# Performance work log

Hardware: AMD Instinct MI355X
Metric: run time of the kernel (lower is better)

## Reference

```python
import jax, jax.numpy as jnp
import numpy as np

B, S, D, H = 4, 1024, 1024, 16
HD = D // H
EPS = 1e-5


def _layernorm(x, g, b):
    m = jnp.mean(x, axis=-1, keepdims=True)
    v = jnp.mean((x - m) ** 2, axis=-1, keepdims=True)
    return (x - m) * jax.lax.rsqrt(v + EPS) * g + b


def setup_inputs() -> dict:
    key = jax.random.key(0)
    ks = jax.random.split(key, 8)
    sc = 1.0 / np.sqrt(D)
    return {
        "x": jax.random.normal(ks[0], (B, S, D), dtype=jnp.float32),
        "seq_len": jax.random.randint(ks[1], (B,), 1, S + 1, dtype=jnp.int32),
        "Wq": jax.random.normal(ks[2], (D, D), dtype=jnp.float32) * sc,
        "bq": jnp.zeros((D,), dtype=jnp.float32),
        "Wk": jax.random.normal(ks[3], (D, D), dtype=jnp.float32) * sc,
        "bk": jnp.zeros((D,), dtype=jnp.float32),
        "Wv": jax.random.normal(ks[4], (D, D), dtype=jnp.float32) * sc,
        "bv": jnp.zeros((D,), dtype=jnp.float32),
        "ln_g": jnp.ones((HD,), dtype=jnp.float32),
        "ln_b": jnp.zeros((HD,), dtype=jnp.float32),
    }


def reference(x, seq_len, Wq, bq, Wk, bk, Wv, bv, ln_g, ln_b):
    # Faithful quirk: k and v are projections of the ALREADY projected q.
    q = x @ Wq.T + bq                      # [B,S,D]
    k = q @ Wk.T + bk
    v = q @ Wv.T + bv
    # [B,S,D] -> [B,H,S,HD]
    def split_heads(t):
        return t.reshape(B, S, H, HD).transpose(0, 2, 1, 3)
    q, k, v = split_heads(q), split_heads(k), split_heads(v)
    # shared per-head LayerNorm over head_dim
    q = _layernorm(q, ln_g, ln_b)
    k = _layernorm(k, ln_g, ln_b)
    v = _layernorm(v, ln_g, ln_b)
    # raw scores (no temperature scaling in the original; temperature=1.0 unused)
    scores = jnp.einsum("bhqd,bhkd->bhqk", q, k)
    # encoder_mask: multiplicative validity mask on key positions, repeated per head
    mask = (jnp.arange(S)[None, :] < seq_len[:, None]).astype(scores.dtype)  # [B,S]
    scores = scores * mask[:, None, None, :]
    attn = jax.nn.softmax(scores, axis=-1)
    # dropout is identity at inference
    out = jnp.einsum("bhqk,bhkd->bhqd", attn, v)
    return out.transpose(0, 2, 1, 3).reshape(B, S, D)
```

## Files before the change

kernel.cpp:

```cpp
#include <hip/hip_runtime.h>

#define B_  4
#define S_  1024
#define D_  1024
#define H_  16
#define HD_ 64
#define EPS_ 1e-5f

typedef _Float16 f16x8 __attribute__((ext_vector_type(8)));
typedef _Float16 f16x4 __attribute__((ext_vector_type(4)));
typedef __bf16 bf16x8 __attribute__((ext_vector_type(8)));
typedef float  f32x4  __attribute__((ext_vector_type(4)));
typedef unsigned short ushort8v __attribute__((ext_vector_type(8)));

static __device__ __forceinline__ unsigned short f2bf(float f) {
  union { float f; unsigned u; } v; v.f = f;
  unsigned r = v.u + 0x7fffu + ((v.u >> 16) & 1u);
  return (unsigned short)(r >> 16);
}
static __device__ __forceinline__ float bf2f(unsigned short u) {
  union { unsigned u; float f; } v; v.u = ((unsigned)u) << 16;
  return v.f;
}

#define GLD16(gp, lp) __builtin_amdgcn_global_load_lds( \
    (const __attribute__((address_space(1))) void*)(gp), \
    (__attribute__((address_space(3))) void*)(lp), 16, 0, 0)

__global__ __launch_bounds__(256) void cvt_all(
    const float* __restrict__ x,  _Float16* __restrict__ xh,
    const float* __restrict__ Wq, _Float16* __restrict__ wqh,
    const float* __restrict__ Wk, _Float16* __restrict__ wkh,
    const float* __restrict__ Wv, _Float16* __restrict__ wvh,
    float* __restrict__ Vtail) {
  int bid = blockIdx.x;
  if (bid >= 7168) {
    int i = (bid - 7168) * 1024 + threadIdx.x * 4;
    *(float4*)(Vtail + i) = make_float4(0.f, 0.f, 0.f, 0.f);
    return;
  }
  const float* src; _Float16* dst; int base;
  if (bid < 4096)      { src = x;  dst = xh;  base = bid; }
  else if (bid < 5120) { src = Wq; dst = wqh; base = bid - 4096; }
  else if (bid < 6144) { src = Wk; dst = wkh; base = bid - 5120; }
  else                 { src = Wv; dst = wvh; base = bid - 6144; }
  int i = base * 1024 + threadIdx.x * 4;
  float4 f = *(const float4*)(src + i);
  f16x4 h;
  h.x = (_Float16)f.x; h.y = (_Float16)f.y; h.z = (_Float16)f.z; h.w = (_Float16)f.w;
  *(f16x4*)(dst + i) = h;
}

__global__ __launch_bounds__(256, 2) void gemm_bt_bias(
    const _Float16* __restrict__ A,
    const _Float16* __restrict__ B0, const float* __restrict__ bias0,
    _Float16* __restrict__ C0,
    const _Float16* __restrict__ B1, const float* __restrict__ bias1,
    _Float16* __restrict__ C1,
    int M, int N, int K)
{
  const _Float16* Bm = blockIdx.z ? B1 : B0;
  const float* bias  = blockIdx.z ? bias1 : bias0;
  _Float16* C        = blockIdx.z ? C1 : C0;

  __shared__ _Float16 As[2 * 128 * 32];
  __shared__ _Float16 Bs[2 * 64 * 32];

  int tid  = threadIdx.x;
  int lane = tid & 63;
  int wave = tid >> 6;
  int wm = wave >> 1, wn = wave & 1;
  int qd = lane >> 4, l15 = lane & 15;

  long row0 = (long)blockIdx.y * 128;
  long col0 = (long)blockIdx.x * 64;

  int r_a = tid >> 2;
  int c_a = (tid & 3) * 8;

  f32x4 acc[4][2] = {};

  for (int kk = 0; kk < K; kk += 64) {
    GLD16(A  + (row0 + r_a) * K + kk + c_a,           As + tid * 8);
    GLD16(A  + (row0 + 64 + r_a) * K + kk + c_a,      As + 2048 + tid * 8);
    GLD16(A  + (row0 + r_a) * K + kk + 32 + c_a,      As + 4096 + tid * 8);
    GLD16(A  + (row0 + 64 + r_a) * K + kk + 32 + c_a, As + 6144 + tid * 8);
    GLD16(Bm + (col0 + r_a) * K + kk + c_a,           Bs + tid * 8);
    GLD16(Bm + (col0 + r_a) * K + kk + 32 + c_a,      Bs + 2048 + tid * 8);
    __syncthreads();

    for (int ks = 0; ks < 2; ks++) {
      f16x8 af[4], bfr[2];
      for (int t = 0; t < 4; t++)
        af[t]  = *(const f16x8*)(As + ks * 4096 + (wm * 64 + t * 16 + l15) * 32 + qd * 8);
      for (int j = 0; j < 2; j++)
        bfr[j] = *(const f16x8*)(Bs + ks * 2048 + (wn * 32 + j * 16 + l15) * 32 + qd * 8);
      for (int i = 0; i < 4; i++)
        for (int j = 0; j < 2; j++)
          acc[i][j] = __builtin_amdgcn_mfma_f32_16x16x32_f16(af[i], bfr[j], acc[i][j], 0, 0, 0);
    }
    __syncthreads();
  }

  for (int i = 0; i < 4; i++) {
    long row = row0 + wm * 64 + i * 16 + qd * 4;
    for (int j = 0; j < 2; j++) {
      long col = col0 + wn * 32 + j * 16 + l15;
      float bv = bias[col];
      for (int r = 0; r < 4; r++)
        C[(row + r) * N + col] = (_Float16)(acc[i][j][r] + bv);
    }
  }
}

__global__ __launch_bounds__(256, 2) void gemm_bt_bias128(
    const _Float16* __restrict__ A,
    const _Float16* __restrict__ B0, const float* __restrict__ bias0,
    _Float16* __restrict__ C0,
    const _Float16* __restrict__ B1, const float* __restrict__ bias1,
    _Float16* __restrict__ C1,
    int M, int N, int K)
{
  const _Float16* Bm = blockIdx.z ? B1 : B0;
  const float* bias  = blockIdx.z ? bias1 : bias0;
  _Float16* C        = blockIdx.z ? C1 : C0;

  __shared__ _Float16 As[2 * 128 * 32];
  __shared__ _Float16 Bs[2 * 128 * 32];

  int tid  = threadIdx.x;
  int lane = tid & 63;
  int wave = tid >> 6;
  int wm = wave >> 1, wn = wave & 1;
  int qd = lane >> 4, l15 = lane & 15;

  long row0 = (long)blockIdx.y * 128;
  long col0 = (long)blockIdx.x * 128;

  int r_a = tid >> 2;
  int c_a = (tid & 3) * 8;

  f32x4 acc[4][4] = {};

  for (int kk = 0; kk < K; kk += 64) {
    GLD16(A  + (row0 + r_a) * K + kk + c_a,           As + tid * 8);
    GLD16(A  + (row0 + 64 + r_a) * K + kk + c_a,      As + 2048 + tid * 8);
    GLD16(A  + (row0 + r_a) * K + kk + 32 + c_a,      As + 4096 + tid * 8);
    GLD16(A  + (row0 + 64 + r_a) * K + kk + 32 + c_a, As + 6144 + tid * 8);
    GLD16(Bm + (col0 + r_a) * K + kk + c_a,           Bs + tid * 8);
    GLD16(Bm + (col0 + 64 + r_a) * K + kk + c_a,      Bs + 2048 + tid * 8);
    GLD16(Bm + (col0 + r_a) * K + kk + 32 + c_a,      Bs + 4096 + tid * 8);
    GLD16(Bm + (col0 + 64 + r_a) * K + kk + 32 + c_a, Bs + 6144 + tid * 8);
    __syncthreads();

    for (int ks = 0; ks < 2; ks++) {
      f16x8 af[4], bfr[4];
      for (int t = 0; t < 4; t++) {
        af[t]  = *(const f16x8*)(As + ks * 4096 + (wm * 64 + t * 16 + l15) * 32 + qd * 8);
        bfr[t] = *(const f16x8*)(Bs + ks * 4096 + (wn * 64 + t * 16 + l15) * 32 + qd * 8);
      }
      for (int i = 0; i < 4; i++)
        for (int j = 0; j < 4; j++)
          acc[i][j] = __builtin_amdgcn_mfma_f32_16x16x32_f16(af[i], bfr[j], acc[i][j], 0, 0, 0);
    }
    __syncthreads();
  }

  for (int i = 0; i < 4; i++) {
    long row = row0 + wm * 64 + i * 16 + qd * 4;
    for (int j = 0; j < 4; j++) {
      long col = col0 + wn * 64 + j * 16 + l15;
      float bv = bias[col];
      for (int r = 0; r < 4; r++)
        C[(row + r) * N + col] = (_Float16)(acc[i][j][r] + bv);
    }
  }
}

__global__ __launch_bounds__(256, 2) void ln_qkv(
    const _Float16* __restrict__ qh,
    const _Float16* __restrict__ kh,
    const _Float16* __restrict__ vh,
    const float* __restrict__ ln_g, const float* __restrict__ ln_b,
    const int* __restrict__ seq_len,
    _Float16* __restrict__ Qn,
    _Float16* __restrict__ Kn,
    unsigned short* __restrict__ Vt,
    float* __restrict__ Vtail)
{
  __shared__ unsigned short Vls[256][68];
  int tid = threadIdx.x;
  int s0 = blockIdx.x * 256;
  int h = blockIdx.y, b = blockIdx.z;
  long bh = (long)b * H_ + h;
  long s = s0 + tid;
  long inbase  = ((long)b * S_ + s) * D_ + (long)h * HD_;
  long outbase = (bh * S_ + s) * HD_;

  f16x8 rw[8];
  {
    for (int i = 0; i < 8; i++) rw[i] = *(const f16x8*)(qh + inbase + i * 8);
    float sum = 0.f, sq = 0.f;
    for (int i = 0; i < 8; i++)
      for (int j = 0; j < 8; j++) { float xv = (float)rw[i][j]; sum += xv; sq = fmaf(xv, xv, sq); }
    float m = sum * (1.f / 64.f);
    float inv = rsqrtf(sq * (1.f / 64.f) - m * m + EPS_);
    for (int i = 0; i < 8; i++) {
      f16x8 o;
      for (int j = 0; j < 8; j++)
        o[j] = (_Float16)(((float)rw[i][j] - m) * inv * ln_g[i * 8 + j] + ln_b[i * 8 + j]);
      *(f16x8*)(Qn + outbase + i * 8) = o;
    }
  }
  {
    for (int i = 0; i < 8; i++) rw[i] = *(const f16x8*)(kh + inbase + i * 8);
    float sum = 0.f, sq = 0.f;
    for (int i = 0; i < 8; i++)
      for (int j = 0; j < 8; j++) { float xv = (float)rw[i][j]; sum += xv; sq = fmaf(xv, xv, sq); }
    float m = sum * (1.f / 64.f);
    float inv = rsqrtf(sq * (1.f / 64.f) - m * m + EPS_);
    for (int i = 0; i < 8; i++) {
      f16x8 o;
      for (int j = 0; j < 8; j++)
        o[j] = (_Float16)(((float)rw[i][j] - m) * inv * ln_g[i * 8 + j] + ln_b[i * 8 + j]);
      *(f16x8*)(Kn + outbase + i * 8) = o;
    }
  }
  {
    for (int i = 0; i < 8; i++) rw[i] = *(const f16x8*)(vh + inbase + i * 8);
    float sum = 0.f, sq = 0.f;
    for (int i = 0; i < 8; i++)
      for (int j = 0; j < 8; j++) { float xv = (float)rw[i][j]; sum += xv; sq = fmaf(xv, xv, sq); }
    float m = sum * (1.f / 64.f);
    float inv = rsqrtf(sq * (1.f / 64.f) - m * m + EPS_);
    for (int i = 0; i < 8; i++)
      for (int j = 0; j < 8; j++)
        Vls[tid][i * 8 + j] = f2bf(((float)rw[i][j] - m) * inv * ln_g[i * 8 + j] + ln_b[i * 8 + j]);
  }
  __syncthreads();
  int d = tid >> 2, sc = tid & 3;
  int len = seq_len[b];
  long vbase = (bh * HD_ + d) * S_ + s0 + sc * 64;
  float tsum = 0.f;
  for (int j0 = 0; j0 < 64; j0 += 8) {
    ushort8v w;
    for (int jj = 0; jj < 8; jj++) {
      unsigned short ub = Vls[sc * 64 + j0 + jj][d];
      w[jj] = ub;
      if (s0 + sc * 64 + j0 + jj >= len) tsum += bf2f(ub);
    }
    *(ushort8v*)(Vt + vbase + j0) = w;
  }
  if (s0 + sc * 64 + 64 > len)
    atomicAdd(&Vtail[bh * HD_ + d], tsum);
}

__global__ __launch_bounds__(256, 2) void attn(
    const _Float16* __restrict__ Qn,
    const _Float16* __restrict__ Kn,
    const unsigned short* __restrict__ Vt,
    const float* __restrict__ Vtail,
    const int* __restrict__ seq_len,
    float* __restrict__ out)
{
  __shared__ _Float16 Ks[2][64 * 32];
  __shared__ unsigned short Vts[2][64 * 32];
  __shared__ unsigned short Ps[4][32 * 72];

  int tid = threadIdx.x, lane = tid & 63, wave = tid >> 6;
  int qd = lane >> 4, l15 = lane & 15;
  int b = blockIdx.x;
  int h = blockIdx.y;
  int q0 = blockIdx.z * 128;
  long bh = (long)b * H_ + h;
  int len = seq_len[b];
  int ntile = (len + 63) >> 6;

  int skey = tid >> 2;
  int schunk = (tid & 3) * 8;

  f16x8 qf[2][2];
  for (int mt = 0; mt < 2; mt++) {
    const _Float16* qp = Qn + (bh * S_ + q0 + wave * 32 + mt * 16 + l15) * HD_;
    qf[mt][0] = *(const f16x8*)(qp + qd * 8);
    qf[mt][1] = *(const f16x8*)(qp + 32 + qd * 8);
  }
  float tv[4];
  for (int t = 0; t < 4; t++) tv[t] = Vtail[bh * HD_ + t * 16 + l15];

  f32x4 o[2][4] = {};
  float den[2][4] = {{0.f,0.f,0.f,0.f},{0.f,0.f,0.f,0.f}};

  for (int kt = 0; kt < ntile; kt++) {
    GLD16(Kn + (bh * S_ + kt * 64 + skey) * HD_ + schunk,      &Ks[0][0] + tid * 8);
    GLD16(Kn + (bh * S_ + kt * 64 + skey) * HD_ + 32 + schunk, &Ks[1][0] + tid * 8);
    GLD16(Vt + (bh * HD_ + skey) * S_ + kt * 64 + schunk,      &Vts[0][0] + tid * 8);
    GLD16(Vt + (bh * HD_ + skey) * S_ + kt * 64 + 32 + schunk, &Vts[1][0] + tid * 8);
    __syncthreads();

    f32x4 sacc[2][4] = {};
    for (int tn = 0; tn < 4; tn++) {
      f16x8 kf0 = *(const f16x8*)(&Ks[0][0] + (tn * 16 + l15) * 32 + qd * 8);
      f16x8 kf1 = *(const f16x8*)(&Ks[1][0] + (tn * 16 + l15) * 32 + qd * 8);
      for (int mt = 0; mt < 2; mt++) {
        sacc[mt][tn] = __builtin_amdgcn_mfma_f32_16x16x32_f16(qf[mt][0], kf0, sacc[mt][tn], 0, 0, 0);
        sacc[mt][tn] = __builtin_amdgcn_mfma_f32_16x16x32_f16(qf[mt][1], kf1, sacc[mt][tn], 0, 0, 0);
      }
    }

    for (int mt = 0; mt < 2; mt++)
      for (int tn = 0; tn < 4; tn++) {
        int kg = kt * 64 + tn * 16 + l15;
        for (int r = 0; r < 4; r++) {
          float p = (kg < len) ? __expf(sacc[mt][tn][r]) : 0.f;
          unsigned short pb = f2bf(p);
          den[mt][r] += bf2f(pb);
          Ps[wave][(mt * 16 + qd * 4 + r) * 72 + tn * 16 + l15] = pb;
        }
      }

    bf16x8 pf[2][2];
    for (int mt = 0; mt < 2; mt++) {
      pf[mt][0] = *(const bf16x8*)(&Ps[wave][(mt * 16 + l15) * 72 + qd * 8]);
      pf[mt][1] = *(const bf16x8*)(&Ps[wave][(mt * 16 + l15) * 72 + 32 + qd * 8]);
    }
    for (int t = 0; t < 4; t++) {
      bf16x8 vf0 = *(const bf16x8*)(&Vts[0][0] + (t * 16 + l15) * 32 + qd * 8);
      bf16x8 vf1 = *(const bf16x8*)(&Vts[1][0] + (t * 16 + l15) * 32 + qd * 8);
      for (int mt = 0; mt < 2; mt++) {
        o[mt][t] = __builtin_amdgcn_mfma_f32_16x16x32_bf16(pf[mt][0], vf0, o[mt][t], 0, 0, 0);
        o[mt][t] = __builtin_amdgcn_mfma_f32_16x16x32_bf16(pf[mt][1], vf1, o[mt][t], 0, 0, 0);
      }
    }
    __syncthreads();
  }

  for (int mt = 0; mt < 2; mt++)
    for (int t = 0; t < 4; t++)
      for (int r = 0; r < 4; r++) o[mt][t][r] += tv[t];

  float tden = (float)(S_ - len);
  for (int mt = 0; mt < 2; mt++)
    for (int r = 0; r < 4; r++) {
      for (int off = 1; off < 16; off <<= 1)
        den[mt][r] += __shfl_xor(den[mt][r], off, 64);
      den[mt][r] += tden;
    }

  for (int mt = 0; mt < 2; mt++)
    for (int t = 0; t < 4; t++)
      for (int r = 0; r < 4; r++) {
        long s = q0 + wave * 32 + mt * 16 + qd * 4 + r;
        long dcol = (long)h * HD_ + t * 16 + l15;
        out[((long)b * S_ + s) * D_ + dcol] = o[mt][t][r] / den[mt][r];
      }
}

extern "C" void kernel_launch(void* const* d_in, const int* in_sizes, int n_in,
                              void* d_out, int out_size, void* d_ws, size_t ws_size,
                              hipStream_t stream) {
  const float* x     = (const float*)d_in[0];
  const int*  seq    = (const int*)d_in[1];
  const float* Wq    = (const float*)d_in[2];
  const float* bq    = (const float*)d_in[3];
  const float* Wk    = (const float*)d_in[4];
  const float* bk    = (const float*)d_in[5];
  const float* Wv    = (const float*)d_in[6];
  const float* bv    = (const float*)d_in[7];
  const float* ln_g  = (const float*)d_in[8];
  const float* ln_b  = (const float*)d_in[9];
  float* out = (float*)d_out;

  char* ws = (char*)d_ws;
  _Float16* xh  = (_Float16*)(ws);
  _Float16* wqh = (_Float16*)(ws + (8l  << 20));
  _Float16* wkh = (_Float16*)(ws + (10l << 20));
  _Float16* wvh = (_Float16*)(ws + (12l << 20));
  float*    Vtail = (float*)(ws + (14l << 20));
  _Float16* qh  = (_Float16*)(ws + (16l << 20));
  _Float16* kh  = (_Float16*)(ws + (24l << 20));
  _Float16* vh  = (_Float16*)(ws + (32l << 20));
  _Float16* Qn  = (_Float16*)(ws + (40l << 20));
  _Float16* Kn  = (_Float16*)(ws + (48l << 20));
  unsigned short* Vt = (unsigned short*)(ws + (56l << 20));

  cvt_all<<<7172, 256, 0, stream>>>(x, xh, Wq, wqh, Wk, wkh, Wv, wvh, Vtail);

  dim3 g1(D_ / 64, (B_ * S_) / 128, 1);
  gemm_bt_bias<<<g1, 256, 0, stream>>>(xh, wqh, bq, qh, wqh, bq, qh,
                                       B_ * S_, D_, D_);
  dim3 g2(D_ / 128, (B_ * S_) / 128, 2);
  gemm_bt_bias128<<<g2, 256, 0, stream>>>(qh, wkh, bk, kh, wvh, bv, vh,
                                          B_ * S_, D_, D_);

  dim3 g3(S_ / 256, H_, B_);
  ln_qkv<<<g3, 256, 0, stream>>>(qh, kh, vh, ln_g, ln_b, seq, Qn, Kn, Vt, Vtail);

  dim3 g4(B_, H_, S_ / 128);
  attn<<<g4, 256, 0, stream>>>(Qn, Kn, Vt, Vtail, seq, out);
}
```

Baseline: 181.7 us.

## Split LN over 4 lanes per row with coalesced LDS-staged loads

Rewrites the per-head LayerNorm kernel so each row is handled by four lanes with shuffle reductions instead of one thread per row, and stages the Q/K/V tiles through shared memory using coalesced 16-byte async loads. Blocks now cover 64 sequence positions rather than 256, giving 4x more blocks and a higher occupancy hint. The aim is to raise parallelism and memory coalescing in a bandwidth-bound stage. In exchange it adds more blocks, more atomics on Vtail, and extra LDS traffic.

```diff
diff --git a/kernel.cpp b/kernel.cpp
--- a/kernel.cpp
+++ b/kernel.cpp
@@ -177,7 +177,7 @@
   }
 }
 
-__global__ __launch_bounds__(256, 2) void ln_qkv(
+__global__ __launch_bounds__(256, 4) void ln_qkv(
     const _Float16* __restrict__ qh,
     const _Float16* __restrict__ kh,
     const _Float16* __restrict__ vh,
@@ -188,70 +188,116 @@
     unsigned short* __restrict__ Vt,
     float* __restrict__ Vtail)
 {
-  __shared__ unsigned short Vls[256][68];
-  int tid = threadIdx.x;
-  int s0 = blockIdx.x * 256;
+  __shared__ _Float16 Qs[2][64 * 32];
+  __shared__ _Float16 Ks_[2][64 * 32];
+  __shared__ _Float16 Vs[2][64 * 32];
+  __shared__ unsigned short Vls[64][68];
+
+  int tid = threadIdx.x, lane = tid & 63, w = tid >> 6;
+  int a = lane >> 4, r16 = lane & 15;
+  int row = w * 16 + r16;
+  int s0 = blockIdx.x * 64;
   int h = blockIdx.y, b = blockIdx.z;
   long bh = (long)b * H_ + h;
-  long s = s0 + tid;
-  long inbase  = ((long)b * S_ + s) * D_ + (long)h * HD_;
-  long outbase = (bh * S_ + s) * HD_;
-
-  f16x8 rw[8];
+  int len = seq_len[b];
+
+  int skey = tid >> 2, schunk = (tid & 3) * 8;
+  long gbase = ((long)b * S_ + s0 + skey) * D_ + (long)h * HD_ + schunk;
+  GLD16(qh + gbase,      &Qs[0][0] + tid * 8);
+  GLD16(qh + gbase + 32, &Qs[1][0] + tid * 8);
+  GLD16(kh + gbase,      &Ks_[0][0] + tid * 8);
+  GLD16(kh + gbase + 32, &Ks_[1][0] + tid * 8);
+  GLD16(vh + gbase,      &Vs[0][0] + tid * 8);
+  GLD16(vh + gbase + 32, &Vs[1][0] + tid * 8);
+
+  float g0[8], bb0[8], g1[8], bb1[8];
+  for (int u = 0; u < 8; u++) {
+    g0[u] = ln_g[a * 8 + u];       bb0[u] = ln_b[a * 8 + u];
+    g1[u] = ln_g[32 + a * 8 + u];  bb1[u] = ln_b[32 + a * 8 + u];
+  }
+  __syncthreads();
+
+  long obase = (bh * S_ + s0 + row) * HD_;
+
   {
-    for (int i = 0; i < 8; i++) rw[i] = *(const f16x8*)(qh + inbase + i * 8);
+    f16x8 x0 = *(const f16x8*)(&Qs[0][row * 32 + a * 8]);
+    f16x8 x1 = *(const f16x8*)(&Qs[1][row * 32 + a * 8]);
     float sum = 0.f, sq = 0.f;
-    for (int i = 0; i < 8; i++)
-      for (int j = 0; j < 8; j++) { float xv = (float)rw[i][j]; sum += xv; sq = fmaf(xv, xv, sq); }
+    for (int u = 0; u < 8; u++) {
+      float v0 = (float)x0[u], v1 = (float)x1[u];
+      sum += v0 + v1; sq = fmaf(v0, v0, fmaf(v1, v1, sq));
+    }
+    for (int off = 16; off < 64; off <<= 1) {
+      sum += __shfl_xor(sum, off, 64); sq += __shfl_xor(sq, off, 64);
+    }
     float m = sum * (1.f / 64.f);
     float inv = rsqrtf(sq * (1.f / 64.f) - m * m + EPS_);
-    for (int i = 0; i < 8; i++) {
-      f16x8 o;
-      for (int j = 0; j < 8; j++)
-        o[j] = (_Float16)(((float)rw[i][j] - m) * inv * ln_g[i * 8 + j] + ln_b[i * 8 + j]);
-      *(f16x8*)(Qn + outbase + i * 8) = o;
-    }
+    f16x8 o0, o1;
+    for (int u = 0; u < 8; u++) {
+      o0[u] = (_Float16)(((float)x0[u] - m) * inv * g0[u] + bb0[u]);
+      o1[u] = (_Float16)(((float)x1[u] - m) * inv * g1[u] + bb1[u]);
+    }
+    *(f16x8*)(Qn + obase + a * 8) = o0;
+    *(f16x8*)(Qn + obase + 32 + a * 8) = o1;
   }
   {
-    for (int i = 0; i < 8; i++) rw[i] = *(const f16x8*)(kh + inbase + i * 8);
+    f16x8 x0 = *(const f16x8*)(&Ks_[0][row * 32 + a * 8]);
+    f16x8 x1 = *(const f16x8*)(&Ks_[1][row * 32 + a * 8]);
     float sum = 0.f, sq = 0.f;
-    for (int i = 0; i < 8; i++)
-      for (int j = 0; j < 8; j++) { float xv = (float)rw[i][j]; sum += xv; sq = fmaf(xv, xv, sq); }
+    for (int u = 0; u < 8; u++) {
+      float v0 = (float)x0[u], v1 = (float)x1[u];
+      sum += v0 + v1; sq = fmaf(v0, v0, fmaf(v1, v1, sq));
+    }
+    for (int off = 16; off < 64; off <<= 1) {
+      sum += __shfl_xor(sum, off, 64); sq += __shfl_xor(sq, off, 64);
+    }
     float m = sum * (1.f / 64.f);
     float inv = rsqrtf(sq * (1.f / 64.f) - m * m + EPS_);
-    for (int i = 0; i < 8; i++) {
-      f16x8 o;
-      for (int j = 0; j < 8; j++)
-        o[j] = (_Float16)(((float)rw[i][j] - m) * inv * ln_g[i * 8 + j] + ln_b[i * 8 + j]);
-      *(f16x8*)(Kn + outbase + i * 8) = o;
-    }
+    f16x8 o0, o1;
+    for (int u = 0; u < 8; u++) {
+      o0[u] = (_Float16)(((float)x0[u] - m) * inv * g0[u] + bb0[u]);
+      o1[u] = (_Float16)(((float)x1[u] - m) * inv * g1[u] + bb1[u]);
+    }
+    *(f16x8*)(Kn + obase + a * 8) = o0;
+    *(f16x8*)(Kn + obase + 32 + a * 8) = o1;
   }
   {
-    for (int i = 0; i < 8; i++) rw[i] = *(const f16x8*)(vh + inbase + i * 8);
+    f16x8 x0 = *(const f16x8*)(&Vs[0][row * 32 + a * 8]);
+    f16x8 x1 = *(const f16x8*)(&Vs[1][row * 32 + a * 8]);
     float sum = 0.f, sq = 0.f;
-    for (int i = 0; i < 8; i++)
-      for (int j = 0; j < 8; j++) { float xv = (float)rw[i][j]; sum += xv; sq = fmaf(xv, xv, sq); }
+    for (int u = 0; u < 8; u++) {
+      float v0 = (float)x0[u], v1 = (float)x1[u];
+      sum += v0 + v1; sq = fmaf(v0, v0, fmaf(v1, v1, sq));
+    }
+    for (int off = 16; off < 64; off <<= 1) {
+      sum += __shfl_xor(sum, off, 64); sq += __shfl_xor(sq, off, 64);
+    }
     float m = sum * (1.f / 64.f);
     float inv = rsqrtf(sq * (1.f / 64.f) - m * m + EPS_);
-    for (int i = 0; i < 8; i++)
-      for (int j = 0; j < 8; j++)
-        Vls[tid][i * 8 + j] = f2bf(((float)rw[i][j] - m) * inv * ln_g[i * 8 + j] + ln_b[i * 8 + j]);
+    for (int u = 0; u < 8; u++) {
+      Vls[row][a * 8 + u]      = f2bf(((float)x0[u] - m) * inv * g0[u] + bb0[u]);
+      Vls[row][32 + a * 8 + u] = f2bf(((float)x1[u] - m) * inv * g1[u] + bb1[u]);
+    }
   }
   __syncthreads();
+
   int d = tid >> 2, sc = tid & 3;
-  int len = seq_len[b];
-  long vbase = (bh * HD_ + d) * S_ + s0 + sc * 64;
+  long vbase = (bh * HD_ + d) * S_ + s0 + sc * 16;
   float tsum = 0.f;
-  for (int j0 = 0; j0 < 64; j0 += 8) {
-    ushort8v w;
-    for (int jj = 0; jj < 8; jj++) {
-      unsigned short ub = Vls[sc * 64 + j0 + jj][d];
-      w[jj] = ub;
-      if (s0 + sc * 64 + j0 + jj >= len) tsum += bf2f(ub);
-    }
-    *(ushort8v*)(Vt + vbase + j0) = w;
-  }
-  if (s0 + sc * 64 + 64 > len)
+  ushort8v w0, w1;
+  for (int j = 0; j < 8; j++) {
+    unsigned short ub = Vls[sc * 16 + j][d];
+    w0[j] = ub;
+    if (s0 + sc * 16 + j >= len) tsum += bf2f(ub);
+  }
+  for (int j = 0; j < 8; j++) {
+    unsigned short ub = Vls[sc * 16 + 8 + j][d];
+    w1[j] = ub;
+    if (s0 + sc * 16 + 8 + j >= len) tsum += bf2f(ub);
+  }
+  *(ushort8v*)(Vt + vbase) = w0;
+  *(ushort8v*)(Vt + vbase + 8) = w1;
+  if (s0 + sc * 16 + 16 > len)
     atomicAdd(&Vtail[bh * HD_ + d], tsum);
 }
 
@@ -393,7 +439,7 @@
   gemm_bt_bias128<<<g2, 256, 0, stream>>>(qh, wkh, bk, kh, wvh, bv, vh,
                                           B_ * S_, D_, D_);
 
-  dim3 g3(S_ / 256, H_, B_);
+  dim3 g3(S_ / 64, H_, B_);
   ln_qkv<<<g3, 256, 0, stream>>>(qh, kh, vh, ln_g, ln_b, seq, Qn, Kn, Vt, Vtail);
 
   dim3 g4(B_, H_, S_ / 128);
```

Result: slower. 188.9 us (+4.0%).
